# Kernel tuning notes

Measured on AMD Instinct MI355X. Metric: run time of the kernel, lower is better.

Reference implementation:

```python
import jax, jax.numpy as jnp
import numpy as np

NB, NA, HD, EF = 16, 128, 256, 30


def setup_inputs() -> dict:
    key = jax.random.key(0)
    ks = jax.random.split(key, 4)
    h = jax.random.normal(ks[0], (NB, NA, HD), dtype=jnp.float32)
    e = jax.random.normal(ks[1], (NB, NA, NA, EF), dtype=jnp.float32)
    node_mask = jnp.ones((NB, NA, 1), dtype=jnp.float32)
    edge_mask = jnp.ones((NB, NA, NA, 1), dtype=jnp.float32)
    Wf = jax.random.normal(ks[2], (HD, EF), dtype=jnp.float32) * (1.0 / np.sqrt(EF))
    bf = jnp.zeros((HD,), dtype=jnp.float32)
    Ww = jax.random.normal(ks[3], (HD, 2 * HD), dtype=jnp.float32) * (1.0 / np.sqrt(2 * HD))
    bw = jnp.zeros((HD,), dtype=jnp.float32)
    return {"h": h, "e": e, "node_mask": node_mask, "edge_mask": edge_mask,
            "Wf": Wf, "bf": bf, "Ww": Ww, "bw": bw}


def reference(h, e, node_mask, edge_mask, Wf, bf, Ww, bw):
    # filter_net: Linear(30->HD) + SELU, then edge mask  -> (nb, na, na, HD)
    e_f = jax.nn.selu(jnp.einsum('bijk,fk->bijf', e, Wf) + bf) * edge_mask
    # h1[b,i,f] = sum_j h[b,j,f] * e_f[b,i,j,f]   (broadcast multiply-reduce over edge dim)
    h1 = jnp.einsum('bjf,bijf->bif', h, e_f)
    # gated node MLP: Linear(2HD->HD) + SELU, node mask, residual
    z = jnp.concatenate([h, h1], axis=-1)  # (nb, na, 2HD)
    h1 = jax.nn.selu(jnp.einsum('bic,fc->bif', z, Ww) + bw) * node_mask
    return h1 + h
```

## Files before the change

### kernel.cpp

```cpp
#include <hip/hip_runtime.h>
#include <hip/hip_bf16.h>

#define NB 16
#define NA 128
#define HD 256
#define EF 30

#define SELU_SCALE 1.0507009873554805f
#define SELU_AS    1.7580993408473766f

typedef __attribute__((ext_vector_type(8))) short bf16x8;
typedef __attribute__((ext_vector_type(4))) float f32x4;

__device__ __forceinline__ unsigned short f2u16(float x) {
    union { __hip_bfloat16 b; unsigned short u; } cv;
    cv.b = __float2bfloat16(x);
    return cv.u;
}
__device__ __forceinline__ short f2s16(float x) { return (short)f2u16(x); }

__device__ __forceinline__ float selu_f(float s) {
    float pos = SELU_SCALE * s;
    float neg = fmaf(SELU_AS, __expf(s), -SELU_AS);
    return s > 0.f ? pos : neg;
}

__global__ __launch_bounds__(256)
void efconv_prep(const float* __restrict__ Wf, const float* __restrict__ Ww,
                 unsigned short* __restrict__ WfFragU, unsigned short* __restrict__ WwFragU)
{
    const int idx = blockIdx.x * 256 + threadIdx.x;
    if (idx < 16*64*8) {
        const int e = idx & 7, lane = (idx >> 3) & 63, t = idx >> 9;
        const int f = t*16 + (lane & 15);
        const int k = ((lane >> 4) << 3) + e;
        const float v = (k < EF) ? Wf[f*EF + k] : 0.f;
        WfFragU[idx] = f2u16(v);
    }
    const int jdx = idx - 16*64*8;
    if (jdx >= 0 && jdx < 16*16*64*8) {
        const int e = jdx & 7, lane = (jdx >> 3) & 63;
        const int s = (jdx >> 9) & 15, t = jdx >> 13;
        const int f = t*16 + (lane & 15);
        const int k = s*32 + ((lane >> 4) << 3) + e;
        WwFragU[jdx] = f2u16(Ww[f*(2*HD) + k]);
    }
}

__global__ __launch_bounds__(256)
void efconv_stage1(const float* __restrict__ e, const float* __restrict__ h,
                   const float* __restrict__ em, const float* __restrict__ bf,
                   const bf16x8* __restrict__ WfFrag, unsigned short* __restrict__ h1b)
{
    const int bi  = blockIdx.x;
    const int b   = bi >> 7;
    const int tid = threadIdx.x;
    const int wid = tid >> 6;
    const int lane = tid & 63;
    const int l15 = lane & 15;
    const int lq  = lane >> 4;
    const int k0  = lq * 8;

    const float* __restrict__ e_row  = e  + (size_t)bi * (NA*EF);
    const float* __restrict__ em_row = em + (size_t)bi * NA;
    const float* __restrict__ hb     = h  + (size_t)b  * (NA*HD);

    bf16x8 Bf[4];
    float bias[4];
#pragma unroll
    for (int n = 0; n < 4; ++n) {
        const int t = wid*4 + n;
        Bf[n]   = WfFrag[t*64 + lane];
        bias[n] = bf[t*16 + l15];
    }

    float partial[4] = {0.f, 0.f, 0.f, 0.f};

    for (int j0 = 0; j0 < NA; j0 += 16) {
        const int j = j0 + l15;
        const float2* __restrict__ ep2 = reinterpret_cast<const float2*>(e_row + j*EF);
        bf16x8 Af;
#pragma unroll
        for (int p = 0; p < 4; ++p) {
            const int kk = k0 + 2*p;
            float2 v;
            if (kk < EF) v = ep2[kk >> 1]; else { v.x = 0.f; v.y = 0.f; }
            Af[2*p]   = f2s16(v.x);
            Af[2*p+1] = f2s16(v.y);
        }
        const int jr = j0 + lq*4;
        float emv[4];
#pragma unroll
        for (int r = 0; r < 4; ++r) emv[r] = em_row[jr + r];

#pragma unroll
        for (int n = 0; n < 4; ++n) {
            f32x4 acc = {bias[n], bias[n], bias[n], bias[n]};
            acc = __builtin_amdgcn_mfma_f32_16x16x32_bf16(Af, Bf[n], acc, 0, 0, 0);
            const int f = (wid*4 + n)*16 + l15;
#pragma unroll
            for (int r = 0; r < 4; ++r) {
                const float efv = selu_f(acc[r]) * emv[r];
                partial[n] = fmaf(hb[(jr + r)*HD + f], efv, partial[n]);
            }
        }
    }
#pragma unroll
    for (int n = 0; n < 4; ++n) {
        partial[n] += __shfl_xor(partial[n], 16);
        partial[n] += __shfl_xor(partial[n], 32);
    }
    if (lane < 16) {
#pragma unroll
        for (int n = 0; n < 4; ++n) {
            const int f = (wid*4 + n)*16 + lane;
            h1b[(size_t)bi*HD + f] = f2u16(partial[n]);
        }
    }
}

__global__ __launch_bounds__(256)
void efconv_stage2(const float* __restrict__ h, const unsigned short* __restrict__ h1b,
                   const float* __restrict__ nm, const float* __restrict__ bw,
                   const bf16x8* __restrict__ WwFrag, float* __restrict__ out)
{
    const int tid  = threadIdx.x;
    const int lane = tid & 63;
    const int wid  = tid >> 6;
    const int wgid = blockIdx.x*4 + wid;
    const int m    = wgid >> 4;
    const int t    = wgid & 15;
    const int l15  = lane & 15;
    const int lq   = lane >> 4;
    const int k0   = lq * 8;
    const int row  = m*16 + l15;

    const float biasv = bw[t*16 + l15];
    f32x4 acc = {biasv, biasv, biasv, biasv};

    const float4* __restrict__ hrow = reinterpret_cast<const float4*>(h + (size_t)row*HD);
#pragma unroll
    for (int s = 0; s < 8; ++s) {
        const int k = s*32 + k0;
        const float4 v0 = hrow[k >> 2];
        const float4 v1 = hrow[(k >> 2) + 1];
        bf16x8 Af;
        Af[0]=f2s16(v0.x); Af[1]=f2s16(v0.y); Af[2]=f2s16(v0.z); Af[3]=f2s16(v0.w);
        Af[4]=f2s16(v1.x); Af[5]=f2s16(v1.y); Af[6]=f2s16(v1.z); Af[7]=f2s16(v1.w);
        const bf16x8 Bfr = WwFrag[(t*16 + s)*64 + lane];
        acc = __builtin_amdgcn_mfma_f32_16x16x32_bf16(Af, Bfr, acc, 0, 0, 0);
    }
    const bf16x8* __restrict__ h1row = reinterpret_cast<const bf16x8*>(h1b + (size_t)row*HD);
#pragma unroll
    for (int s = 8; s < 16; ++s) {
        const int k = s*32 + k0 - 256;
        const bf16x8 Af = h1row[k >> 3];
        const bf16x8 Bfr = WwFrag[(t*16 + s)*64 + lane];
        acc = __builtin_amdgcn_mfma_f32_16x16x32_bf16(Af, Bfr, acc, 0, 0, 0);
    }

    const int f = t*16 + l15;
#pragma unroll
    for (int r = 0; r < 4; ++r) {
        const int bi = m*16 + lq*4 + r;
        const float v = selu_f(acc[r]);
        out[(size_t)bi*HD + f] = fmaf(v, nm[bi], h[(size_t)bi*HD + f]);
    }
}

extern "C" void kernel_launch(void* const* d_in, const int* in_sizes, int n_in,
                              void* d_out, int out_size, void* d_ws, size_t ws_size,
                              hipStream_t stream)
{
    (void)in_sizes; (void)n_in; (void)out_size; (void)ws_size;
    const float* h  = (const float*)d_in[0];
    const float* e  = (const float*)d_in[1];
    const float* nm = (const float*)d_in[2];
    const float* em = (const float*)d_in[3];
    const float* Wf = (const float*)d_in[4];
    const float* bf = (const float*)d_in[5];
    const float* Ww = (const float*)d_in[6];
    const float* bw = (const float*)d_in[7];
    float* out = (float*)d_out;

    unsigned short* h1b     = (unsigned short*)d_ws;
    unsigned short* WfFragU = (unsigned short*)((char*)d_ws + (1u << 20));
    unsigned short* WwFragU = (unsigned short*)((char*)d_ws + (1u << 20) + 16384);

    hipLaunchKernelGGL(efconv_prep, dim3(544), dim3(256), 0, stream,
                       Wf, Ww, WfFragU, WwFragU);
    hipLaunchKernelGGL(efconv_stage1, dim3(NB * NA), dim3(256), 0, stream,
                       e, h, em, bf, (const bf16x8*)WfFragU, h1b);
    hipLaunchKernelGGL(efconv_stage2, dim3(512), dim3(256), 0, stream,
                       h, h1b, nm, bw, (const bf16x8*)WwFragU, out);
}
```

Baseline: 116.4 us.

## Stage edge rows in LDS and pre-pack h/h1 into MFMA fragment layout

Stage1 now copies each block's 128x30 edge row into shared memory with coalesced float4 loads before building MFMA A-fragments, replacing strided per-lane global float2 loads. The prep kernel additionally converts h into a bf16 fragment-ordered buffer, and stage1 writes h1 directly in fragment order, so stage2 loads A-fragments as single contiguous bf16x8 reads without conversion. Occupancy hint set to 4 blocks per SM. The trade-off is that the prep kernel grows substantially (2592 blocks converting all of h) and stage1 adds an LDS round trip and a barrier.

```diff
diff --git a/kernel.cpp b/kernel.cpp
--- a/kernel.cpp
+++ b/kernel.cpp
@@ -25,17 +25,20 @@
     return s > 0.f ? pos : neg;
 }
 
+
 __global__ __launch_bounds__(256)
 void efconv_prep(const float* __restrict__ Wf, const float* __restrict__ Ww,
-                 unsigned short* __restrict__ WfFragU, unsigned short* __restrict__ WwFragU)
+                 const float* __restrict__ h,
+                 unsigned short* __restrict__ WfFragU,
+                 unsigned short* __restrict__ WwFragU,
+                 unsigned short* __restrict__ hAU)
 {
     const int idx = blockIdx.x * 256 + threadIdx.x;
     if (idx < 16*64*8) {
         const int e = idx & 7, lane = (idx >> 3) & 63, t = idx >> 9;
         const int f = t*16 + (lane & 15);
         const int k = ((lane >> 4) << 3) + e;
-        const float v = (k < EF) ? Wf[f*EF + k] : 0.f;
-        WfFragU[idx] = f2u16(v);
+        WfFragU[idx] = f2u16((k < EF) ? Wf[f*EF + k] : 0.f);
     }
     const int jdx = idx - 16*64*8;
     if (jdx >= 0 && jdx < 16*16*64*8) {
@@ -45,25 +48,39 @@
         const int k = s*32 + ((lane >> 4) << 3) + e;
         WwFragU[jdx] = f2u16(Ww[f*(2*HD) + k]);
     }
-}
-
-__global__ __launch_bounds__(256)
+    const int kdx = idx - 16*64*8 - 16*16*64*8;
+    if (kdx >= 0 && kdx < 128*8*64*8) {
+        const int e = kdx & 7, lane = (kdx >> 3) & 63;
+        const int s = (kdx >> 9) & 7, m = kdx >> 12;
+        const int row = m*16 + (lane & 15);
+        const int k = s*32 + ((lane >> 4) << 3) + e;
+        hAU[kdx] = f2u16(h[row*HD + k]);
+    }
+}
+
+__global__ __launch_bounds__(256, 4)
 void efconv_stage1(const float* __restrict__ e, const float* __restrict__ h,
                    const float* __restrict__ em, const float* __restrict__ bf,
-                   const bf16x8* __restrict__ WfFrag, unsigned short* __restrict__ h1b)
-{
-    const int bi  = blockIdx.x;
-    const int b   = bi >> 7;
-    const int tid = threadIdx.x;
-    const int wid = tid >> 6;
+                   const bf16x8* __restrict__ WfFrag,
+                   unsigned short* __restrict__ h1A)
+{
+    __shared__ float elds[NA * EF];
+
+    const int bi   = blockIdx.x;
+    const int b    = bi >> 7;
+    const int tid  = threadIdx.x;
+    const int wid  = tid >> 6;
     const int lane = tid & 63;
-    const int l15 = lane & 15;
-    const int lq  = lane >> 4;
-    const int k0  = lq * 8;
-
-    const float* __restrict__ e_row  = e  + (size_t)bi * (NA*EF);
-    const float* __restrict__ em_row = em + (size_t)bi * NA;
-    const float* __restrict__ hb     = h  + (size_t)b  * (NA*HD);
+    const int l15  = lane & 15;
+    const int lq   = lane >> 4;
+    const int k0   = lq * 8;
+
+    {
+        const float4* __restrict__ src = reinterpret_cast<const float4*>(e + (size_t)bi * (NA*EF));
+        float4* dst = reinterpret_cast<float4*>(elds);
+        for (int it = tid; it < 960; it += 256) dst[it] = src[it];
+    }
+    __syncthreads();
 
     bf16x8 Bf[4];
     float bias[4];
@@ -74,20 +91,27 @@
         bias[n] = bf[t*16 + l15];
     }
 
+    const float* __restrict__ em_row = em + (size_t)bi * NA;
+    const float* __restrict__ hb     = h  + (size_t)b  * (NA*HD);
+    const bool ktail = (k0 == 24);
+
     float partial[4] = {0.f, 0.f, 0.f, 0.f};
 
     for (int j0 = 0; j0 < NA; j0 += 16) {
         const int j = j0 + l15;
-        const float2* __restrict__ ep2 = reinterpret_cast<const float2*>(e_row + j*EF);
+        const float* __restrict__ ep = elds + j*EF + k0;
+        const float2 v0 = *reinterpret_cast<const float2*>(ep + 0);
+        const float2 v1 = *reinterpret_cast<const float2*>(ep + 2);
+        const float2 v2 = *reinterpret_cast<const float2*>(ep + 4);
+        const float2 vt = *reinterpret_cast<const float2*>(ep + (ktail ? 4 : 6));
+        const float v6 = ktail ? 0.f : vt.x;
+        const float v7 = ktail ? 0.f : vt.y;
         bf16x8 Af;
-#pragma unroll
-        for (int p = 0; p < 4; ++p) {
-            const int kk = k0 + 2*p;
-            float2 v;
-            if (kk < EF) v = ep2[kk >> 1]; else { v.x = 0.f; v.y = 0.f; }
-            Af[2*p]   = f2s16(v.x);
-            Af[2*p+1] = f2s16(v.y);
-        }
+        Af[0] = f2s16(v0.x); Af[1] = f2s16(v0.y);
+        Af[2] = f2s16(v1.x); Af[3] = f2s16(v1.y);
+        Af[4] = f2s16(v2.x); Af[5] = f2s16(v2.y);
+        Af[6] = f2s16(v6);   Af[7] = f2s16(v7);
+
         const int jr = j0 + lq*4;
         float emv[4];
 #pragma unroll
@@ -105,6 +129,7 @@
             }
         }
     }
+
 #pragma unroll
     for (int n = 0; n < 4; ++n) {
         partial[n] += __shfl_xor(partial[n], 16);
@@ -114,15 +139,17 @@
 #pragma unroll
         for (int n = 0; n < 4; ++n) {
             const int f = (wid*4 + n)*16 + lane;
-            h1b[(size_t)bi*HD + f] = f2u16(partial[n]);
+            const int idx = ((((bi >> 4)*8 + (f >> 5))*64) + ((f >> 3) & 3)*16 + (bi & 15))*8 + (f & 7);
+            h1A[idx] = f2u16(partial[n]);
         }
     }
 }
 
 __global__ __launch_bounds__(256)
-void efconv_stage2(const float* __restrict__ h, const unsigned short* __restrict__ h1b,
-                   const float* __restrict__ nm, const float* __restrict__ bw,
-                   const bf16x8* __restrict__ WwFrag, float* __restrict__ out)
+void efconv_stage2(const float* __restrict__ h, const bf16x8* __restrict__ hA,
+                   const bf16x8* __restrict__ h1A, const float* __restrict__ nm,
+                   const float* __restrict__ bw, const bf16x8* __restrict__ WwFrag,
+                   float* __restrict__ out)
 {
     const int tid  = threadIdx.x;
     const int lane = tid & 63;
@@ -132,30 +159,20 @@
     const int t    = wgid & 15;
     const int l15  = lane & 15;
     const int lq   = lane >> 4;
-    const int k0   = lq * 8;
-    const int row  = m*16 + l15;
 
     const float biasv = bw[t*16 + l15];
     f32x4 acc = {biasv, biasv, biasv, biasv};
 
-    const float4* __restrict__ hrow = reinterpret_cast<const float4*>(h + (size_t)row*HD);
 #pragma unroll
     for (int s = 0; s < 8; ++s) {
-        const int k = s*32 + k0;
-        const float4 v0 = hrow[k >> 2];
-        const float4 v1 = hrow[(k >> 2) + 1];
-        bf16x8 Af;
-        Af[0]=f2s16(v0.x); Af[1]=f2s16(v0.y); Af[2]=f2s16(v0.z); Af[3]=f2s16(v0.w);
-        Af[4]=f2s16(v1.x); Af[5]=f2s16(v1.y); Af[6]=f2s16(v1.z); Af[7]=f2s16(v1.w);
+        const bf16x8 Af  = hA[(m*8 + s)*64 + lane];
         const bf16x8 Bfr = WwFrag[(t*16 + s)*64 + lane];
         acc = __builtin_amdgcn_mfma_f32_16x16x32_bf16(Af, Bfr, acc, 0, 0, 0);
     }
-    const bf16x8* __restrict__ h1row = reinterpret_cast<const bf16x8*>(h1b + (size_t)row*HD);
-#pragma unroll
-    for (int s = 8; s < 16; ++s) {
-        const int k = s*32 + k0 - 256;
-        const bf16x8 Af = h1row[k >> 3];
-        const bf16x8 Bfr = WwFrag[(t*16 + s)*64 + lane];
+#pragma unroll
+    for (int s = 0; s < 8; ++s) {
+        const bf16x8 Af  = h1A[(m*8 + s)*64 + lane];
+        const bf16x8 Bfr = WwFrag[(t*16 + s + 8)*64 + lane];
         acc = __builtin_amdgcn_mfma_f32_16x16x32_bf16(Af, Bfr, acc, 0, 0, 0);
     }
 
@@ -183,14 +200,16 @@
     const float* bw = (const float*)d_in[7];
     float* out = (float*)d_out;
 
-    unsigned short* h1b     = (unsigned short*)d_ws;
+    unsigned short* h1A     = (unsigned short*)d_ws;
     unsigned short* WfFragU = (unsigned short*)((char*)d_ws + (1u << 20));
-    unsigned short* WwFragU = (unsigned short*)((char*)d_ws + (1u << 20) + 16384);
-
-    hipLaunchKernelGGL(efconv_prep, dim3(544), dim3(256), 0, stream,
-                       Wf, Ww, WfFragU, WwFragU);
+    unsigned short* WwFragU = (unsigned short*)((char*)d_ws + (1u << 20) + (16u << 10));
+    unsigned short* hAU     = (unsigned short*)((char*)d_ws + (1u << 20) + (272u << 10));
+
+    hipLaunchKernelGGL(efconv_prep, dim3(2592), dim3(256), 0, stream,
+                       Wf, Ww, h, WfFragU, WwFragU, hAU);
     hipLaunchKernelGGL(efconv_stage1, dim3(NB * NA), dim3(256), 0, stream,
-                       e, h, em, bf, (const bf16x8*)WfFragU, h1b);
+                       e, h, em, bf, (const bf16x8*)WfFragU, h1A);
     hipLaunchKernelGGL(efconv_stage2, dim3(512), dim3(256), 0, stream,
-                       h, h1b, nm, bw, (const bf16x8*)WwFragU, out);
-}
+                       h, (const bf16x8*)hAU, (const bf16x8*)h1A, nm, bw,
+                       (const bf16x8*)WwFragU, out);
+}
```

Measured after the change: 117.5 us. No clear change (+0.9%).
